# Kernel tuning notes

Hardware: AMD Instinct MI355X
Metric: run time of the kernel (lower is better)

Reference implementation:

```python
import jax, jax.numpy as jnp
import numpy as np


def setup_inputs() -> dict:
    key = jax.random.key(0)
    k0, k1, k2, k3, k4 = jax.random.split(key, 5)
    B, S, D, F, E = 2, 1024, 1024, 2048, 8
    x = jax.random.normal(k0, (B, S, D), dtype=jnp.float32)
    router_weight = jax.random.normal(k1, (D, E), dtype=jnp.float32) * (1.0 / np.sqrt(D))
    std_in = (1.0 / np.sqrt(3.0)) / np.sqrt(D)   # fan_in = d_model for w1/w2
    std_out = (1.0 / np.sqrt(3.0)) / np.sqrt(F)  # fan_in = d_ff for w3
    w1 = jax.random.normal(k2, (E, D, F), dtype=jnp.float32) * std_in
    w2 = jax.random.normal(k3, (E, D, F), dtype=jnp.float32) * std_in
    w3 = jax.random.normal(k4, (E, F, D), dtype=jnp.float32) * std_out
    return {"x": x, "router_weight": router_weight, "w1": w1, "w2": w2, "w3": w3, "top_k": 2}


def reference(x, router_weight, w1, w2, w3, top_k):
    B, S, D = x.shape
    E = w1.shape[0]
    xf = x.reshape(-1, D)                         # (T, D), T = B*S
    T = xf.shape[0]
    # Router: linear + softmax + top-k, then renormalize top-k weights
    logits = xf @ router_weight                   # (T, E)
    probs = jax.nn.softmax(logits, axis=-1)
    topk_w, topk_idx = jax.lax.top_k(probs, top_k)  # (T, k)
    topk_w = topk_w / jnp.sum(topk_w, axis=-1, keepdims=True)
    # Dense combine weights: cw[t, e] = routing weight if expert e selected for token t, else 0
    cw = jnp.zeros((T, E), dtype=xf.dtype).at[jnp.arange(T)[:, None], topk_idx].add(topk_w)
    # Expert SwiGLU: loop over small fixed expert count (structurally distinct weights)
    out = jnp.zeros_like(xf)
    for e in range(E):
        h = jax.nn.silu(xf @ w1[e]) * (xf @ w2[e])  # (T, F)
        out = out + cw[:, e:e + 1] * (h @ w3[e])    # (T, D)
    return out.reshape(B, S, D)
```

## Files before the change

kernel.cpp:

```cpp
#include <hip/hip_runtime.h>
#include <hip/hip_bf16.h>
#include <stdint.h>

#define T_TOK 2048
#define DMODEL 1024
#define FDIM 2048
#define NEXP 8
#define MAXS 40

typedef __bf16 bf16;
typedef __attribute__((ext_vector_type(8))) __bf16 bf16x8;
typedef __attribute__((ext_vector_type(4))) float f32x4;

#define GLOBAL_AS __attribute__((address_space(1)))
#define LDS_AS __attribute__((address_space(3)))
#define VMCNT(n) asm volatile("s_waitcnt vmcnt(" #n ")" ::: "memory")
#define GLD16(src, dst) __builtin_amdgcn_global_load_lds((const GLOBAL_AS void*)(src), (LDS_AS void*)(dst), 16, 0, 0)

#define XG_SLOT   131072u
#define H_SLOT    262144u
#define W_SLAB    2097152u

__global__ __launch_bounds__(64) void moe_router(
    const float* __restrict__ x, const float* __restrict__ rw,
    bf16* __restrict__ xb, int* __restrict__ counts,
    int* __restrict__ tok_list, float* __restrict__ wgt_list)
{
  const int t = blockIdx.x;
  const int lane = threadIdx.x;
  const float* xr = x + (size_t)t * DMODEL;
  float acc[NEXP];
#pragma unroll
  for (int e = 0; e < NEXP; ++e) acc[e] = 0.f;
  for (int d = lane; d < DMODEL; d += 64) {
    float xv = xr[d];
    if (xb) xb[(size_t)t * DMODEL + d] = (bf16)xv;
    const float* r = rw + (size_t)d * NEXP;
#pragma unroll
    for (int e = 0; e < NEXP; ++e) acc[e] += xv * r[e];
  }
#pragma unroll
  for (int e = 0; e < NEXP; ++e) {
#pragma unroll
    for (int off = 32; off >= 1; off >>= 1)
      acc[e] += __shfl_xor(acc[e], off, 64);
  }
  if (lane == 0) {
    int i0 = 0; float m0 = acc[0];
#pragma unroll
    for (int e = 1; e < NEXP; ++e) { if (acc[e] > m0) { m0 = acc[e]; i0 = e; } }
    int i1 = -1; float m1 = -3.402823466e38f;
#pragma unroll
    for (int e = 0; e < NEXP; ++e) { if (e != i0 && acc[e] > m1) { m1 = acc[e]; i1 = e; } }
    float r = expf(m1 - m0);
    float w0 = 1.f / (1.f + r);
    float w1v = r / (1.f + r);
    int p0 = atomicAdd(&counts[i0], 1);
    tok_list[i0 * T_TOK + p0] = t;
    wgt_list[i0 * T_TOK + p0] = w0;
    int p1 = atomicAdd(&counts[i1], 1);
    tok_list[i1 * T_TOK + p1] = t;
    wgt_list[i1 * T_TOK + p1] = w1v;
  }
}

__global__ void moe_prefix(const int* __restrict__ counts, int* __restrict__ base,
                           int* __restrict__ sched)
{
  if (threadIdx.x == 0) {
    int s = 0, i = 0;
    for (int e = 0; e < NEXP; ++e) {
      base[e] = s; s += counts[e];
      const int nt = (counts[e] + 127) / 128;
      for (int tt = 0; tt < nt; ++tt) sched[i++] = (e << 16) | tt;
    }
    for (; i < MAXS; ++i) sched[i] = -1;
  }
}

__global__ __launch_bounds__(256) void moe_gather(
    const float* __restrict__ x, const int* __restrict__ tok_list,
    const int* __restrict__ counts, const int* __restrict__ sched,
    bf16* __restrict__ xg)
{
  const int s = sched[blockIdx.x];
  if (s < 0) return;
  const int e = s >> 16, tt = s & 0xffff;
  int rem = counts[e] - tt * 128; if (rem > 128) rem = 128;
  const int w = threadIdx.x >> 6, lane = threadIdx.x & 63;
  const int r = blockIdx.y * 4 + w;
  const int rc = r < rem ? r : rem - 1;
  const int tok = tok_list[e * T_TOK + tt * 128 + rc];
  const float* xr = x + (size_t)tok * DMODEL + lane * 16;
  f32x4 v0 = *(const f32x4*)(xr);
  f32x4 v1 = *(const f32x4*)(xr + 4);
  f32x4 v2 = *(const f32x4*)(xr + 8);
  f32x4 v3 = *(const f32x4*)(xr + 12);
  bf16x8 a, b;
#pragma unroll
  for (int j = 0; j < 4; ++j) { a[j] = (bf16)v0[j]; a[4 + j] = (bf16)v1[j]; }
#pragma unroll
  for (int j = 0; j < 4; ++j) { b[j] = (bf16)v2[j]; b[4 + j] = (bf16)v3[j]; }
  bf16* dst = xg + (size_t)blockIdx.x * XG_SLOT + (size_t)(lane * 2) * 1024 + r * 8;
  *(bf16x8*)dst = a;
  *(bf16x8*)(dst + 1024) = b;
}

__global__ __launch_bounds__(256) void transpose_blk12(
    const float* __restrict__ w1, const float* __restrict__ w2,
    bf16* __restrict__ w1b, bf16* __restrict__ w2b)
{
  const int C = FDIM;
  __shared__ float tile[64][65];
  const int z = blockIdx.z;
  const int e = z & 7;
  const float* inp = (z < 8 ? w1 : w2) + (size_t)e * DMODEL * FDIM;
  bf16* outp = (z < 8 ? w1b : w2b) + (size_t)e * W_SLAB;
  const int rb = blockIdx.y * 64;
  const int cb = blockIdx.x * 64;
  const int tid = threadIdx.x;
  const int r = tid >> 2, c0 = (tid & 3) * 16;
  const float* src = inp + (size_t)(rb + r) * C + (cb + c0);
#pragma unroll
  for (int j = 0; j < 16; j += 4) {
    f32x4 v = *(const f32x4*)(src + j);
    tile[r][c0 + j + 0] = v[0];
    tile[r][c0 + j + 1] = v[1];
    tile[r][c0 + j + 2] = v[2];
    tile[r][c0 + j + 3] = v[3];
  }
  __syncthreads();
  bf16x8 a, b;
#pragma unroll
  for (int j = 0; j < 8; ++j) a[j] = (bf16)tile[c0 + j][r];
#pragma unroll
  for (int j = 0; j < 8; ++j) b[j] = (bf16)tile[c0 + 8 + j][r];
  const int ft = blockIdx.x;
  const int ktd = blockIdx.y * 2 + c0 / 32;
  const int kc = (c0 & 31) / 8;
  bf16* dst = outp + ((size_t)ft * 128 + ktd * 4 + kc) * 512 + r * 8;
  *(bf16x8*)dst = a;
  *(bf16x8*)(dst + 512) = b;
}

__global__ __launch_bounds__(256) void transpose_blk3(
    const float* __restrict__ w3, bf16* __restrict__ w3b)
{
  const int C = DMODEL;
  __shared__ float tile[64][65];
  const int e = blockIdx.z;
  const float* inp = w3 + (size_t)e * FDIM * DMODEL;
  bf16* outp = w3b + (size_t)e * W_SLAB;
  const int rb = blockIdx.y * 64;
  const int cb = blockIdx.x * 64;
  const int tid = threadIdx.x;
  const int r = tid >> 2, c0 = (tid & 3) * 16;
  const float* src = inp + (size_t)(rb + r) * C + (cb + c0);
#pragma unroll
  for (int j = 0; j < 16; j += 4) {
    f32x4 v = *(const f32x4*)(src + j);
    tile[r][c0 + j + 0] = v[0];
    tile[r][c0 + j + 1] = v[1];
    tile[r][c0 + j + 2] = v[2];
    tile[r][c0 + j + 3] = v[3];
  }
  __syncthreads();
  bf16x8 a, b;
#pragma unroll
  for (int j = 0; j < 8; ++j) a[j] = (bf16)tile[c0 + j][r];
#pragma unroll
  for (int j = 0; j < 8; ++j) b[j] = (bf16)tile[c0 + 8 + j][r];
  const int dt = blockIdx.x;
  const int ktf = blockIdx.y * 2 + c0 / 32;
  const int kc = (c0 & 31) / 8;
  bf16* dst = outp + ((size_t)dt * 256 + ktf * 4 + kc) * 512 + r * 8;
  *(bf16x8*)dst = a;
  *(bf16x8*)(dst + 512) = b;
}

__global__ __launch_bounds__(256) void moe_gemm1_blk(
    const bf16* __restrict__ xg,
    const bf16* __restrict__ w1b, const bf16* __restrict__ w2b,
    const int* __restrict__ counts, const int* __restrict__ sched,
    bf16* __restrict__ hblk)
{
  const int s = sched[blockIdx.y];
  if (s < 0) return;
  const int e = s >> 16, tt = s & 0xffff;
  int rem = counts[e] - tt * 128; if (rem > 128) rem = 128;
  const int ft = blockIdx.x;

  __shared__ __align__(16) bf16 As[3][4][128][8];
  __shared__ __align__(16) bf16 Ws[3][2][4][64][8];

  const int tid = threadIdx.x;
  const int lane = tid & 63;
  const int w = tid >> 6;
  const int wr = w >> 1, wc = w & 1;
  const int lh = lane >> 4, ll = lane & 15;

  const bf16* axg = xg + (size_t)blockIdx.y * XG_SLOT + w * 1024 + lane * 8;
  const bf16* w1e = w1b + (size_t)e * W_SLAB + ((size_t)ft * 128 + w) * 512 + lane * 8;
  const bf16* w2e = w2b + (size_t)e * W_SLAB + ((size_t)ft * 128 + w) * 512 + lane * 8;

  f32x4 acc1[4][2], acc2[4][2];
  const f32x4 fz = {0.f, 0.f, 0.f, 0.f};
#pragma unroll
  for (int mf = 0; mf < 4; ++mf)
#pragma unroll
    for (int nf = 0; nf < 2; ++nf) { acc1[mf][nf] = fz; acc2[mf][nf] = fz; }

#define STAGE1(B, KT)                                              \
  {                                                                \
    GLD16(axg + (size_t)(KT) * 4096,       &As[B][w][0][0]);       \
    GLD16(axg + (size_t)(KT) * 4096 + 512, &As[B][w][64][0]);      \
    GLD16(w1e + (size_t)(KT) * 2048,       &Ws[B][0][w][0][0]);    \
    GLD16(w2e + (size_t)(KT) * 2048,       &Ws[B][1][w][0][0]);    \
  }

  const int NT = DMODEL / 32;
  STAGE1(0, 0);
  STAGE1(1, 1);
  VMCNT(4);
  __builtin_amdgcn_s_barrier();

  int ld = 0;
  for (int t = 0; t < NT; ++t) {
    int pf = ld + 2; if (pf >= 3) pf -= 3;
    if (t + 2 < NT) STAGE1(pf, t + 2);

    bf16x8 af[4], b1[2], b2[2];
#pragma unroll
    for (int mf = 0; mf < 4; ++mf)
      af[mf] = *(const bf16x8*)&As[ld][lh][wr * 64 + mf * 16 + ll][0];
#pragma unroll
    for (int nf = 0; nf < 2; ++nf) {
      b1[nf] = *(const bf16x8*)&Ws[ld][0][lh][wc * 32 + nf * 16 + ll][0];
      b2[nf] = *(const bf16x8*)&Ws[ld][1][lh][wc * 32 + nf * 16 + ll][0];
    }
    __builtin_amdgcn_s_setprio(1);
#pragma unroll
    for (int mf = 0; mf < 4; ++mf)
#pragma unroll
      for (int nf = 0; nf < 2; ++nf) {
        acc1[mf][nf] = __builtin_amdgcn_mfma_f32_16x16x32_bf16(af[mf], b1[nf], acc1[mf][nf], 0, 0, 0);
        acc2[mf][nf] = __builtin_amdgcn_mfma_f32_16x16x32_bf16(af[mf], b2[nf], acc2[mf][nf], 0, 0, 0);
      }
    __builtin_amdgcn_s_setprio(0);

    if (t + 2 < NT)      { VMCNT(4); __builtin_amdgcn_s_barrier(); }
    else if (t + 1 < NT) { VMCNT(0); __builtin_amdgcn_s_barrier(); }
    ld = (ld + 1 == 3) ? 0 : ld + 1;
  }
#undef STAGE1

  bf16* hs = hblk + (size_t)blockIdx.y * H_SLOT;
  const int kth = ft * 2 + wc;
#pragma unroll
  for (int mf = 0; mf < 4; ++mf)
#pragma unroll
    for (int nf = 0; nf < 2; ++nf) {
      const int kch = nf * 2 + (ll >> 3);
      bf16* hp = hs + ((size_t)kth * 4 + kch) * 1024 + (ll & 7);
#pragma unroll
      for (int r = 0; r < 4; ++r) {
        const int rl = wr * 64 + mf * 16 + lh * 4 + r;
        if (rl < rem) {
          const float a = acc1[mf][nf][r];
          const float b = acc2[mf][nf][r];
          const float h = (a / (1.f + expf(-a))) * b;
          hp[rl * 8] = (bf16)h;
        }
      }
    }
}

__global__ __launch_bounds__(256) void moe_gemm2_blk(
    const bf16* __restrict__ hblk, const bf16* __restrict__ w3b,
    const int* __restrict__ tok_list, const float* __restrict__ wgt_list,
    const int* __restrict__ counts, const int* __restrict__ sched,
    float* __restrict__ out)
{
  const int s = sched[blockIdx.y];
  if (s < 0) return;
  const int e = s >> 16, tt = s & 0xffff;
  int rem = counts[e] - tt * 128; if (rem > 128) rem = 128;
  const int dtb = blockIdx.x;
  const int kz = blockIdx.z;

  __shared__ __align__(16) bf16 As[3][4][128][8];
  __shared__ __align__(16) bf16 Ws[3][4][128][8];
  __shared__ int toks[128];
  __shared__ float wgts[128];

  const int tid = threadIdx.x;
  const int lane = tid & 63;
  const int w = tid >> 6;
  const int wr = w >> 1, wc = w & 1;
  const int lh = lane >> 4, ll = lane & 15;

  if (tid < 128) {
    int r = tid < rem ? tid : rem - 1;
    toks[tid] = tok_list[e * T_TOK + tt * 128 + r];
    wgts[tid] = wgt_list[e * T_TOK + tt * 128 + r];
  }
  __syncthreads();

  const bf16* ah = hblk + (size_t)blockIdx.y * H_SLOT + (size_t)kz * 131072 + w * 1024 + lane * 8;
  const int fh = w & 1;
  const int kcp = (w >> 1) << 1;
  const bf16* w3w = w3b + (size_t)e * W_SLAB
      + ((size_t)(2 * dtb + fh) * 256 + (size_t)kz * 128 + kcp) * 512 + lane * 8;

  f32x4 acc[4][4];
  const f32x4 fz = {0.f, 0.f, 0.f, 0.f};
#pragma unroll
  for (int mf = 0; mf < 4; ++mf)
#pragma unroll
    for (int nf = 0; nf < 4; ++nf) acc[mf][nf] = fz;

#define STAGE2(B, KT)                                                    \
  {                                                                      \
    GLD16(ah  + (size_t)(KT) * 4096,       &As[B][w][0][0]);             \
    GLD16(ah  + (size_t)(KT) * 4096 + 512, &As[B][w][64][0]);            \
    GLD16(w3w + (size_t)(KT) * 2048,       &Ws[B][kcp][fh * 64][0]);     \
    GLD16(w3w + (size_t)(KT) * 2048 + 512, &Ws[B][kcp + 1][fh * 64][0]); \
  }

  const int NT = (FDIM / 2) / 32;
  STAGE2(0, 0);
  STAGE2(1, 1);
  VMCNT(4);
  __builtin_amdgcn_s_barrier();

  int ld = 0;
  for (int t = 0; t < NT; ++t) {
    int pf = ld + 2; if (pf >= 3) pf -= 3;
    if (t + 2 < NT) STAGE2(pf, t + 2);

    bf16x8 af[4], bv[4];
#pragma unroll
    for (int mf = 0; mf < 4; ++mf)
      af[mf] = *(const bf16x8*)&As[ld][lh][wr * 64 + mf * 16 + ll][0];
#pragma unroll
    for (int nf = 0; nf < 4; ++nf)
      bv[nf] = *(const bf16x8*)&Ws[ld][lh][wc * 64 + nf * 16 + ll][0];
    __builtin_amdgcn_s_setprio(1);
#pragma unroll
    for (int mf = 0; mf < 4; ++mf)
#pragma unroll
      for (int nf = 0; nf < 4; ++nf)
        acc[mf][nf] = __builtin_amdgcn_mfma_f32_16x16x32_bf16(af[mf], bv[nf], acc[mf][nf], 0, 0, 0);
    __builtin_amdgcn_s_setprio(0);

    if (t + 2 < NT)      { VMCNT(4); __builtin_amdgcn_s_barrier(); }
    else if (t + 1 < NT) { VMCNT(0); __builtin_amdgcn_s_barrier(); }
    ld = (ld + 1 == 3) ? 0 : ld + 1;
  }
#undef STAGE2

#pragma unroll
  for (int mf = 0; mf < 4; ++mf)
#pragma unroll
    for (int nf = 0; nf < 4; ++nf)
#pragma unroll
      for (int r = 0; r < 4; ++r) {
        const int rl = wr * 64 + mf * 16 + lh * 4 + r;
        if (rl < rem) {
          const int col = dtb * 128 + wc * 64 + nf * 16 + ll;
          atomicAdd(&out[(size_t)toks[rl] * DMODEL + col], acc[mf][nf][r] * wgts[rl]);
        }
      }
}

__global__ __launch_bounds__(256, 2) void moe_gemm1(
    const bf16* __restrict__ xb,
    const float* __restrict__ w1, const float* __restrict__ w2,
    const int* __restrict__ tok_list, const int* __restrict__ counts,
    const int* __restrict__ base, bf16* __restrict__ H)
{
  const int e = blockIdx.z;
  const int tt = blockIdx.y;
  const int ft = blockIdx.x;
  const int cnt = counts[e];
  if (tt * 128 >= cnt) return;
  int rem = cnt - tt * 128; if (rem > 128) rem = 128;

  __shared__ __align__(16) bf16 As[4][128][8];
  __shared__ __align__(16) bf16 Ws[2][4][64][8];
  __shared__ int toks[128];

  const int tid = threadIdx.x;
  const int lane = tid & 63;
  const int w = tid >> 6;
  const int wr = w >> 1, wc = w & 1;
  const int lh = lane >> 4, ll = lane & 15;

  if (tid < 128) {
    int r = tid < rem ? tid : rem - 1;
    toks[tid] = tok_list[e * T_TOK + tt * 128 + r];
  }
  __syncthreads();

  f32x4 acc1[4][2], acc2[4][2];
  const f32x4 fz = {0.f, 0.f, 0.f, 0.f};
#pragma unroll
  for (int mf = 0; mf < 4; ++mf)
#pragma unroll
    for (int nf = 0; nf < 2; ++nf) { acc1[mf][nf] = fz; acc2[mf][nf] = fz; }

  const float* w1e = w1 + (size_t)e * DMODEL * FDIM + ft * 64;
  const float* w2e = w2 + (size_t)e * DMODEL * FDIM + ft * 64;
  const int sf = tid & 63;
  const int skc = tid >> 6;

  for (int k0 = 0; k0 < DMODEL; k0 += 32) {
    __syncthreads();
#pragma unroll
    for (int i = 0; i < 2; ++i) {
      const int c = w + i * 4;
      const int kc = c >> 1;
      const int rh = c & 1;
      const int row = rh * 64 + lane;
      GLD16(xb + (size_t)toks[row] * DMODEL + (k0 + kc * 8), &As[kc][rh * 64][0]);
    }
    {
      const size_t rowoff = (size_t)(k0 + skc * 8) * FDIM + sf;
      const float* s1 = w1e + rowoff;
      const float* s2 = w2e + rowoff;
      bf16x8 v1, v2;
#pragma unroll
      for (int j = 0; j < 8; ++j) {
        v1[j] = (bf16)s1[(size_t)j * FDIM];
        v2[j] = (bf16)s2[(size_t)j * FDIM];
      }
      *(bf16x8*)&Ws[0][skc][sf][0] = v1;
      *(bf16x8*)&Ws[1][skc][sf][0] = v2;
    }
    __syncthreads();
    bf16x8 af[4];
#pragma unroll
    for (int mf = 0; mf < 4; ++mf)
      af[mf] = *(const bf16x8*)&As[lh][wr * 64 + mf * 16 + ll][0];
    bf16x8 b1[2], b2[2];
#pragma unroll
    for (int nf = 0; nf < 2; ++nf) {
      b1[nf] = *(const bf16x8*)&Ws[0][lh][wc * 32 + nf * 16 + ll][0];
      b2[nf] = *(const bf16x8*)&Ws[1][lh][wc * 32 + nf * 16 + ll][0];
    }
#pragma unroll
    for (int mf = 0; mf < 4; ++mf)
#pragma unroll
      for (int nf = 0; nf < 2; ++nf) {
        acc1[mf][nf] = __builtin_amdgcn_mfma_f32_16x16x32_bf16(af[mf], b1[nf], acc1[mf][nf], 0, 0, 0);
        acc2[mf][nf] = __builtin_amdgcn_mfma_f32_16x16x32_bf16(af[mf], b2[nf], acc2[mf][nf], 0, 0, 0);
      }
  }

  const int hbase = base[e] + tt * 128;
#pragma unroll
  for (int mf = 0; mf < 4; ++mf)
#pragma unroll
    for (int nf = 0; nf < 2; ++nf)
#pragma unroll
      for (int r = 0; r < 4; ++r) {
        const int rl = wr * 64 + mf * 16 + lh * 4 + r;
        if (rl < rem) {
          const int fg = ft * 64 + wc * 32 + nf * 16 + ll;
          const float a = acc1[mf][nf][r];
          const float b = acc2[mf][nf][r];
          const float h = (a / (1.f + expf(-a))) * b;
          H[(size_t)(hbase + rl) * FDIM + fg] = (bf16)h;
        }
      }
}

__global__ __launch_bounds__(256, 2) void moe_gemm2(
    const bf16* __restrict__ H, const float* __restrict__ w3,
    const int* __restrict__ tok_list, const float* __restrict__ wgt_list,
    const int* __restrict__ counts, const int* __restrict__ base,
    float* __restrict__ out)
{
  const int e = blockIdx.z;
  const int tt = blockIdx.y;
  const int dt = blockIdx.x;
  const int cnt = counts[e];
  if (tt * 128 >= cnt) return;
  int rem = cnt - tt * 128; if (rem > 128) rem = 128;

  __shared__ __align__(16) bf16 As[4][128][8];
  __shared__ __align__(16) bf16 Ws[4][64][8];
  __shared__ int toks[128];
  __shared__ float wgts[128];

  const int tid = threadIdx.x;
  const int lane = tid & 63;
  const int w = tid >> 6;
  const int wr = w >> 1, wc = w & 1;
  const int lh = lane >> 4, ll = lane & 15;

  if (tid < 128) {
    int r = tid < rem ? tid : rem - 1;
    toks[tid] = tok_list[e * T_TOK + tt * 128 + r];
    wgts[tid] = wgt_list[e * T_TOK + tt * 128 + r];
  }
  __syncthreads();

  f32x4 acc[4][2];
  const f32x4 fz = {0.f, 0.f, 0.f, 0.f};
#pragma unroll
  for (int mf = 0; mf < 4; ++mf)
#pragma unroll
    for (int nf = 0; nf < 2; ++nf) acc[mf][nf] = fz;

  const int hbase = base[e] + tt * 128;
  const float* w3e = w3 + (size_t)e * FDIM * DMODEL + dt * 64;
  const int sf = tid & 63;
  const int skc = tid >> 6;

  for (int k0 = 0; k0 < FDIM; k0 += 32) {
    __syncthreads();
#pragma unroll
    for (int i = 0; i < 2; ++i) {
      const int c = w + i * 4;
      const int kc = c >> 1;
      const int rh = c & 1;
      int row = rh * 64 + lane;
      if (row >= rem) row = rem - 1;
      GLD16(H + (size_t)(hbase + row) * FDIM + (k0 + kc * 8), &As[kc][rh * 64][0]);
    }
    {
      const size_t rowoff = (size_t)(k0 + skc * 8) * DMODEL + sf;
      const float* s3 = w3e + rowoff;
      bf16x8 v;
#pragma unroll
      for (int j = 0; j < 8; ++j) v[j] = (bf16)s3[(size_t)j * DMODEL];
      *(bf16x8*)&Ws[skc][sf][0] = v;
    }
    __syncthreads();
    bf16x8 af[4];
#pragma unroll
    for (int mf = 0; mf < 4; ++mf)
      af[mf] = *(const bf16x8*)&As[lh][wr * 64 + mf * 16 + ll][0];
    bf16x8 bv[2];
#pragma unroll
    for (int nf = 0; nf < 2; ++nf)
      bv[nf] = *(const bf16x8*)&Ws[lh][wc * 32 + nf * 16 + ll][0];
#pragma unroll
    for (int mf = 0; mf < 4; ++mf)
#pragma unroll
      for (int nf = 0; nf < 2; ++nf)
        acc[mf][nf] = __builtin_amdgcn_mfma_f32_16x16x32_bf16(af[mf], bv[nf], acc[mf][nf], 0, 0, 0);
  }

#pragma unroll
  for (int mf = 0; mf < 4; ++mf)
#pragma unroll
    for (int nf = 0; nf < 2; ++nf)
#pragma unroll
      for (int r = 0; r < 4; ++r) {
        const int rl = wr * 64 + mf * 16 + lh * 4 + r;
        if (rl < rem) {
          const int col = dt * 64 + wc * 32 + nf * 16 + ll;
          atomicAdd(&out[(size_t)toks[rl] * DMODEL + col], acc[mf][nf][r] * wgts[rl]);
        }
      }
}

extern "C" void kernel_launch(void* const* d_in, const int* in_sizes, int n_in,
                              void* d_out, int out_size, void* d_ws, size_t ws_size,
                              hipStream_t stream)
{
  const float* x  = (const float*)d_in[0];
  const float* rw = (const float*)d_in[1];
  const float* w1 = (const float*)d_in[2];
  const float* w2 = (const float*)d_in[3];
  const float* w3 = (const float*)d_in[4];
  float* out = (float*)d_out;
  char* ws = (char*)d_ws;

  size_t off = 0;
  auto take = [&](size_t bytes) -> char* {
    char* p = ws + off;
    off = (off + bytes + 255) & ~(size_t)255;
    return p;
  };
  int* tok_list   = (int*)take((size_t)NEXP * T_TOK * sizeof(int));
  float* wgt_list = (float*)take((size_t)NEXP * T_TOK * sizeof(float));
  int* counts     = (int*)take(64);
  int* base       = (int*)take(64);
  int* sched      = (int*)take(MAXS * sizeof(int));
  bf16* xg        = (bf16*)take((size_t)MAXS * XG_SLOT * sizeof(bf16));
  bf16* hblk      = (bf16*)take((size_t)MAXS * H_SLOT * sizeof(bf16));
  bf16* w1b       = (bf16*)take((size_t)NEXP * W_SLAB * sizeof(bf16));
  bf16* w2b       = (bf16*)take((size_t)NEXP * W_SLAB * sizeof(bf16));
  bf16* w3b       = (bf16*)take((size_t)NEXP * W_SLAB * sizeof(bf16));
  const bool fast = (ws_size >= off);

  hipMemsetAsync(d_out, 0, (size_t)out_size * sizeof(float), stream);
  hipMemsetAsync(counts, 0, NEXP * sizeof(int), stream);

  if (fast) {
    moe_router<<<dim3(T_TOK), dim3(64), 0, stream>>>(x, rw, nullptr, counts, tok_list, wgt_list);
    moe_prefix<<<dim3(1), dim3(64), 0, stream>>>(counts, base, sched);
    transpose_blk12<<<dim3(FDIM / 64, DMODEL / 64, 2 * NEXP), dim3(256), 0, stream>>>(w1, w2, w1b, w2b);
    transpose_blk3<<<dim3(DMODEL / 64, FDIM / 64, NEXP), dim3(256), 0, stream>>>(w3, w3b);
    moe_gather<<<dim3(MAXS, 32), dim3(256), 0, stream>>>(x, tok_list, counts, sched, xg);
    moe_gemm1_blk<<<dim3(FDIM / 64, MAXS), dim3(256), 0, stream>>>(
        xg, w1b, w2b, counts, sched, hblk);
    moe_gemm2_blk<<<dim3(DMODEL / 128, MAXS, 2), dim3(256), 0, stream>>>(
        hblk, w3b, tok_list, wgt_list, counts, sched, out);
  } else {
    size_t foff = 0;
    auto ftake = [&](size_t bytes) -> char* {
      char* p = ws + foff;
      foff = (foff + bytes + 255) & ~(size_t)255;
      return p;
    };
    int* ftok   = (int*)ftake((size_t)NEXP * T_TOK * sizeof(int));
    float* fwgt = (float*)ftake((size_t)NEXP * T_TOK * sizeof(float));
    int* fcnt   = (int*)ftake(64);
    int* fbase  = (int*)ftake(64);
    int* fsched = (int*)ftake(MAXS * sizeof(int));
    bf16* xb    = (bf16*)ftake((size_t)T_TOK * DMODEL * sizeof(bf16));
    bf16* H     = (bf16*)ftake((size_t)2 * T_TOK * FDIM * sizeof(bf16));
    hipMemsetAsync(fcnt, 0, NEXP * sizeof(int), stream);
    moe_router<<<dim3(T_TOK), dim3(64), 0, stream>>>(x, rw, xb, fcnt, ftok, fwgt);
    moe_prefix<<<dim3(1), dim3(64), 0, stream>>>(fcnt, fbase, fsched);
    moe_gemm1<<<dim3(FDIM / 64, T_TOK / 128, NEXP), dim3(256), 0, stream>>>(
        xb, w1, w2, ftok, fcnt, fbase, H);
    moe_gemm2<<<dim3(DMODEL / 64, T_TOK / 128, NEXP), dim3(256), 0, stream>>>(
        H, w3, ftok, fwgt, fcnt, fbase, out);
  }
}
```

Measured before the change: 245.8 us.

## Fuse fp32 weight conversion into GEMM kernels, drop separate transpose passes

Removes the two transpose/convert kernels that rewrote all expert weights into a blocked bf16 layout every call. Instead, each GEMM block loads fp32 weight tiles into registers, converts them to bf16 and writes them into a swizzled, padded LDS buffer that is double-buffered alongside the async activation loads. This avoids a full read/write pass over roughly 200MB of weights and two launches. The cost is that each weight tile is now read as fp32 (twice the bytes) by every token tile that uses it, and B fragments are gathered from LDS as scalar bf16 loads instead of vector loads.

Measured after the change: 292.3 us. 18.9% more time.

```diff
diff --git a/kernel.cpp b/kernel.cpp
--- a/kernel.cpp
+++ b/kernel.cpp
@@ -15,11 +15,11 @@
 #define GLOBAL_AS __attribute__((address_space(1)))
 #define LDS_AS __attribute__((address_space(3)))
 #define VMCNT(n) asm volatile("s_waitcnt vmcnt(" #n ")" ::: "memory")
+#define LGKM0    asm volatile("s_waitcnt lgkmcnt(0)" ::: "memory")
 #define GLD16(src, dst) __builtin_amdgcn_global_load_lds((const GLOBAL_AS void*)(src), (LDS_AS void*)(dst), 16, 0, 0)
 
 #define XG_SLOT   131072u
 #define H_SLOT    262144u
-#define W_SLAB    2097152u
 
 __global__ __launch_bounds__(64) void moe_router(
     const float* __restrict__ x, const float* __restrict__ rw,
@@ -106,81 +106,9 @@
   *(bf16x8*)(dst + 1024) = b;
 }
 
-__global__ __launch_bounds__(256) void transpose_blk12(
-    const float* __restrict__ w1, const float* __restrict__ w2,
-    bf16* __restrict__ w1b, bf16* __restrict__ w2b)
-{
-  const int C = FDIM;
-  __shared__ float tile[64][65];
-  const int z = blockIdx.z;
-  const int e = z & 7;
-  const float* inp = (z < 8 ? w1 : w2) + (size_t)e * DMODEL * FDIM;
-  bf16* outp = (z < 8 ? w1b : w2b) + (size_t)e * W_SLAB;
-  const int rb = blockIdx.y * 64;
-  const int cb = blockIdx.x * 64;
-  const int tid = threadIdx.x;
-  const int r = tid >> 2, c0 = (tid & 3) * 16;
-  const float* src = inp + (size_t)(rb + r) * C + (cb + c0);
-#pragma unroll
-  for (int j = 0; j < 16; j += 4) {
-    f32x4 v = *(const f32x4*)(src + j);
-    tile[r][c0 + j + 0] = v[0];
-    tile[r][c0 + j + 1] = v[1];
-    tile[r][c0 + j + 2] = v[2];
-    tile[r][c0 + j + 3] = v[3];
-  }
-  __syncthreads();
-  bf16x8 a, b;
-#pragma unroll
-  for (int j = 0; j < 8; ++j) a[j] = (bf16)tile[c0 + j][r];
-#pragma unroll
-  for (int j = 0; j < 8; ++j) b[j] = (bf16)tile[c0 + 8 + j][r];
-  const int ft = blockIdx.x;
-  const int ktd = blockIdx.y * 2 + c0 / 32;
-  const int kc = (c0 & 31) / 8;
-  bf16* dst = outp + ((size_t)ft * 128 + ktd * 4 + kc) * 512 + r * 8;
-  *(bf16x8*)dst = a;
-  *(bf16x8*)(dst + 512) = b;
-}
-
-__global__ __launch_bounds__(256) void transpose_blk3(
-    const float* __restrict__ w3, bf16* __restrict__ w3b)
-{
-  const int C = DMODEL;
-  __shared__ float tile[64][65];
-  const int e = blockIdx.z;
-  const float* inp = w3 + (size_t)e * FDIM * DMODEL;
-  bf16* outp = w3b + (size_t)e * W_SLAB;
-  const int rb = blockIdx.y * 64;
-  const int cb = blockIdx.x * 64;
-  const int tid = threadIdx.x;
-  const int r = tid >> 2, c0 = (tid & 3) * 16;
-  const float* src = inp + (size_t)(rb + r) * C + (cb + c0);
-#pragma unroll
-  for (int j = 0; j < 16; j += 4) {
-    f32x4 v = *(const f32x4*)(src + j);
-    tile[r][c0 + j + 0] = v[0];
-    tile[r][c0 + j + 1] = v[1];
-    tile[r][c0 + j + 2] = v[2];
-    tile[r][c0 + j + 3] = v[3];
-  }
-  __syncthreads();
-  bf16x8 a, b;
-#pragma unroll
-  for (int j = 0; j < 8; ++j) a[j] = (bf16)tile[c0 + j][r];
-#pragma unroll
-  for (int j = 0; j < 8; ++j) b[j] = (bf16)tile[c0 + 8 + j][r];
-  const int dt = blockIdx.x;
-  const int ktf = blockIdx.y * 2 + c0 / 32;
-  const int kc = (c0 & 31) / 8;
-  bf16* dst = outp + ((size_t)dt * 256 + ktf * 4 + kc) * 512 + r * 8;
-  *(bf16x8*)dst = a;
-  *(bf16x8*)(dst + 512) = b;
-}
-
 __global__ __launch_bounds__(256) void moe_gemm1_blk(
     const bf16* __restrict__ xg,
-    const bf16* __restrict__ w1b, const bf16* __restrict__ w2b,
+    const float* __restrict__ w1, const float* __restrict__ w2,
     const int* __restrict__ counts, const int* __restrict__ sched,
     bf16* __restrict__ hblk)
 {
@@ -191,7 +119,7 @@
   const int ft = blockIdx.x;
 
   __shared__ __align__(16) bf16 As[3][4][128][8];
-  __shared__ __align__(16) bf16 Ws[3][2][4][64][8];
+  __shared__ __align__(16) bf16 Wraw[2][2][32][72];
 
   const int tid = threadIdx.x;
   const int lane = tid & 63;
@@ -200,8 +128,15 @@
   const int lh = lane >> 4, ll = lane & 15;
 
   const bf16* axg = xg + (size_t)blockIdx.y * XG_SLOT + w * 1024 + lane * 8;
-  const bf16* w1e = w1b + (size_t)e * W_SLAB + ((size_t)ft * 128 + w) * 512 + lane * 8;
-  const bf16* w2e = w2b + (size_t)e * W_SLAB + ((size_t)ft * 128 + w) * 512 + lane * 8;
+
+  const int wm  = tid >> 7;
+  const int wrk = (tid & 127) >> 2;
+  const int wfc = (tid & 3) << 4;
+  const int wfx = wfc ^ ((wrk >> 3) << 4);
+  const float* wsrc = (wm ? w2 : w1) + (size_t)e * DMODEL * FDIM
+      + (size_t)wrk * FDIM + ft * 64 + wfc;
+
+  f32x4 wv0, wv1, wv2, wv3;
 
   f32x4 acc1[4][2], acc2[4][2];
   const f32x4 fz = {0.f, 0.f, 0.f, 0.f};
@@ -210,49 +145,78 @@
 #pragma unroll
     for (int nf = 0; nf < 2; ++nf) { acc1[mf][nf] = fz; acc2[mf][nf] = fz; }
 
-#define STAGE1(B, KT)                                              \
-  {                                                                \
-    GLD16(axg + (size_t)(KT) * 4096,       &As[B][w][0][0]);       \
-    GLD16(axg + (size_t)(KT) * 4096 + 512, &As[B][w][64][0]);      \
-    GLD16(w1e + (size_t)(KT) * 2048,       &Ws[B][0][w][0][0]);    \
-    GLD16(w2e + (size_t)(KT) * 2048,       &Ws[B][1][w][0][0]);    \
+#define WISSUE1(KT)                                                  \
+  {                                                                  \
+    const float* p_ = wsrc + (size_t)(KT) * (32 * FDIM);             \
+    wv0 = *(const f32x4*)p_;        wv1 = *(const f32x4*)(p_ + 4);   \
+    wv2 = *(const f32x4*)(p_ + 8);  wv3 = *(const f32x4*)(p_ + 12);  \
+  }
+#define WWRITE1(B)                                                   \
+  {                                                                  \
+    bf16x8 lo_, hi_;                                                 \
+    _Pragma("unroll") for (int j = 0; j < 4; ++j) {                  \
+      lo_[j] = (bf16)wv0[j]; lo_[4 + j] = (bf16)wv1[j];              \
+      hi_[j] = (bf16)wv2[j]; hi_[4 + j] = (bf16)wv3[j];              \
+    }                                                                \
+    bf16* d_ = &Wraw[B][wm][wrk][wfx];                               \
+    *(bf16x8*)d_ = lo_;  *(bf16x8*)(d_ + 8) = hi_;                   \
+  }
+#define STAGEA1(B, KT)                                               \
+  {                                                                  \
+    GLD16(axg + (size_t)(KT) * 4096,       &As[B][w][0][0]);         \
+    GLD16(axg + (size_t)(KT) * 4096 + 512, &As[B][w][64][0]);        \
+  }
+#define COMPUTE1(LA, LW)                                                         \
+  {                                                                              \
+    bf16x8 af[4], b1v[2], b2v[2];                                                \
+    _Pragma("unroll") for (int mf = 0; mf < 4; ++mf)                             \
+      af[mf] = *(const bf16x8*)&As[LA][lh][wr * 64 + mf * 16 + ll][0];           \
+    _Pragma("unroll") for (int nf = 0; nf < 2; ++nf) {                           \
+      const int fp_ = (((wc << 1) | nf) ^ lh) * 16 + ll;                         \
+      _Pragma("unroll") for (int j = 0; j < 8; ++j) {                            \
+        b1v[nf][j] = Wraw[LW][0][8 * lh + j][fp_];                               \
+        b2v[nf][j] = Wraw[LW][1][8 * lh + j][fp_];                               \
+      }                                                                          \
+    }                                                                            \
+    __builtin_amdgcn_s_setprio(1);                                               \
+    _Pragma("unroll") for (int mf = 0; mf < 4; ++mf)                             \
+      _Pragma("unroll") for (int nf = 0; nf < 2; ++nf) {                         \
+        acc1[mf][nf] = __builtin_amdgcn_mfma_f32_16x16x32_bf16(af[mf], b1v[nf], acc1[mf][nf], 0, 0, 0); \
+        acc2[mf][nf] = __builtin_amdgcn_mfma_f32_16x16x32_bf16(af[mf], b2v[nf], acc2[mf][nf], 0, 0, 0); \
+      }                                                                          \
+    __builtin_amdgcn_s_setprio(0);                                               \
   }
 
   const int NT = DMODEL / 32;
-  STAGE1(0, 0);
-  STAGE1(1, 1);
-  VMCNT(4);
+  WISSUE1(0);
+  STAGEA1(0, 0);
+  STAGEA1(1, 1);
+  VMCNT(2);
+  WWRITE1(0);
+  LGKM0;
   __builtin_amdgcn_s_barrier();
 
   int ld = 0;
   for (int t = 0; t < NT; ++t) {
+    if (t + 1 < NT) WISSUE1(t + 1);
     int pf = ld + 2; if (pf >= 3) pf -= 3;
-    if (t + 2 < NT) STAGE1(pf, t + 2);
-
-    bf16x8 af[4], b1[2], b2[2];
-#pragma unroll
-    for (int mf = 0; mf < 4; ++mf)
-      af[mf] = *(const bf16x8*)&As[ld][lh][wr * 64 + mf * 16 + ll][0];
-#pragma unroll
-    for (int nf = 0; nf < 2; ++nf) {
-      b1[nf] = *(const bf16x8*)&Ws[ld][0][lh][wc * 32 + nf * 16 + ll][0];
-      b2[nf] = *(const bf16x8*)&Ws[ld][1][lh][wc * 32 + nf * 16 + ll][0];
-    }
-    __builtin_amdgcn_s_setprio(1);
-#pragma unroll
-    for (int mf = 0; mf < 4; ++mf)
-#pragma unroll
-      for (int nf = 0; nf < 2; ++nf) {
-        acc1[mf][nf] = __builtin_amdgcn_mfma_f32_16x16x32_bf16(af[mf], b1[nf], acc1[mf][nf], 0, 0, 0);
-        acc2[mf][nf] = __builtin_amdgcn_mfma_f32_16x16x32_bf16(af[mf], b2[nf], acc2[mf][nf], 0, 0, 0);
-      }
-    __builtin_amdgcn_s_setprio(0);
-
-    if (t + 2 < NT)      { VMCNT(4); __builtin_amdgcn_s_barrier(); }
-    else if (t + 1 < NT) { VMCNT(0); __builtin_amdgcn_s_barrier(); }
+    if (t + 2 < NT) STAGEA1(pf, t + 2);
+
+    COMPUTE1(ld, t & 1);
+
+    if (t + 2 < NT)      { VMCNT(2); }
+    else if (t + 1 < NT) { VMCNT(0); }
+    if (t + 1 < NT) {
+      WWRITE1((t + 1) & 1);
+      LGKM0;
+      __builtin_amdgcn_s_barrier();
+    }
     ld = (ld + 1 == 3) ? 0 : ld + 1;
   }
-#undef STAGE1
+#undef WISSUE1
+#undef WWRITE1
+#undef STAGEA1
+#undef COMPUTE1
 
   bf16* hs = hblk + (size_t)blockIdx.y * H_SLOT;
   const int kth = ft * 2 + wc;
@@ -276,7 +240,7 @@
 }
 
 __global__ __launch_bounds__(256) void moe_gemm2_blk(
-    const bf16* __restrict__ hblk, const bf16* __restrict__ w3b,
+    const bf16* __restrict__ hblk, const float* __restrict__ w3,
     const int* __restrict__ tok_list, const float* __restrict__ wgt_list,
     const int* __restrict__ counts, const int* __restrict__ sched,
     float* __restrict__ out)
@@ -289,7 +253,7 @@
   const int kz = blockIdx.z;
 
   __shared__ __align__(16) bf16 As[3][4][128][8];
-  __shared__ __align__(16) bf16 Ws[3][4][128][8];
+  __shared__ __align__(16) bf16 Wraw[2][32][136];
   __shared__ int toks[128];
   __shared__ float wgts[128];
 
@@ -307,10 +271,14 @@
   __syncthreads();
 
   const bf16* ah = hblk + (size_t)blockIdx.y * H_SLOT + (size_t)kz * 131072 + w * 1024 + lane * 8;
-  const int fh = w & 1;
-  const int kcp = (w >> 1) << 1;
-  const bf16* w3w = w3b + (size_t)e * W_SLAB
-      + ((size_t)(2 * dtb + fh) * 256 + (size_t)kz * 128 + kcp) * 512 + lane * 8;
+
+  const int wrk = tid >> 3;
+  const int wfc = (tid & 7) << 4;
+  const int wfx = wfc ^ ((wrk >> 3) << 4);
+  const float* wsrc = w3 + (size_t)e * FDIM * DMODEL
+      + (size_t)(kz * (FDIM / 2) + wrk) * DMODEL + dtb * 128 + wfc;
+
+  f32x4 wv0, wv1, wv2, wv3;
 
   f32x4 acc[4][4];
   const f32x4 fz = {0.f, 0.f, 0.f, 0.f};
@@ -319,45 +287,74 @@
 #pragma unroll
     for (int nf = 0; nf < 4; ++nf) acc[mf][nf] = fz;
 
-#define STAGE2(B, KT)                                                    \
-  {                                                                      \
-    GLD16(ah  + (size_t)(KT) * 4096,       &As[B][w][0][0]);             \
-    GLD16(ah  + (size_t)(KT) * 4096 + 512, &As[B][w][64][0]);            \
-    GLD16(w3w + (size_t)(KT) * 2048,       &Ws[B][kcp][fh * 64][0]);     \
-    GLD16(w3w + (size_t)(KT) * 2048 + 512, &Ws[B][kcp + 1][fh * 64][0]); \
+#define WISSUE2(KT)                                                  \
+  {                                                                  \
+    const float* p_ = wsrc + (size_t)(KT) * (32 * DMODEL);           \
+    wv0 = *(const f32x4*)p_;        wv1 = *(const f32x4*)(p_ + 4);   \
+    wv2 = *(const f32x4*)(p_ + 8);  wv3 = *(const f32x4*)(p_ + 12);  \
+  }
+#define WWRITE2(B)                                                   \
+  {                                                                  \
+    bf16x8 lo_, hi_;                                                 \
+    _Pragma("unroll") for (int j = 0; j < 4; ++j) {                  \
+      lo_[j] = (bf16)wv0[j]; lo_[4 + j] = (bf16)wv1[j];              \
+      hi_[j] = (bf16)wv2[j]; hi_[4 + j] = (bf16)wv3[j];              \
+    }                                                                \
+    bf16* d_ = &Wraw[B][wrk][wfx];                                   \
+    *(bf16x8*)d_ = lo_;  *(bf16x8*)(d_ + 8) = hi_;                   \
+  }
+#define STAGEA2(B, KT)                                               \
+  {                                                                  \
+    GLD16(ah + (size_t)(KT) * 4096,       &As[B][w][0][0]);          \
+    GLD16(ah + (size_t)(KT) * 4096 + 512, &As[B][w][64][0]);         \
+  }
+#define COMPUTE2(LA, LW)                                                         \
+  {                                                                              \
+    bf16x8 af[4], bv[4];                                                         \
+    _Pragma("unroll") for (int mf = 0; mf < 4; ++mf)                             \
+      af[mf] = *(const bf16x8*)&As[LA][lh][wr * 64 + mf * 16 + ll][0];           \
+    _Pragma("unroll") for (int nf = 0; nf < 4; ++nf) {                           \
+      const int fp_ = (((wc << 2) | nf) ^ lh) * 16 + ll;                         \
+      _Pragma("unroll") for (int j = 0; j < 8; ++j)                              \
+        bv[nf][j] = Wraw[LW][8 * lh + j][fp_];                                   \
+    }                                                                            \
+    __builtin_amdgcn_s_setprio(1);                                               \
+    _Pragma("unroll") for (int mf = 0; mf < 4; ++mf)                             \
+      _Pragma("unroll") for (int nf = 0; nf < 4; ++nf)                           \
+        acc[mf][nf] = __builtin_amdgcn_mfma_f32_16x16x32_bf16(af[mf], bv[nf], acc[mf][nf], 0, 0, 0); \
+    __builtin_amdgcn_s_setprio(0);                                               \
   }
 
   const int NT = (FDIM / 2) / 32;
-  STAGE2(0, 0);
-  STAGE2(1, 1);
-  VMCNT(4);
+  WISSUE2(0);
+  STAGEA2(0, 0);
+  STAGEA2(1, 1);
+  VMCNT(2);
+  WWRITE2(0);
+  LGKM0;
   __builtin_amdgcn_s_barrier();
 
   int ld = 0;
   for (int t = 0; t < NT; ++t) {
+    if (t + 1 < NT) WISSUE2(t + 1);
     int pf = ld + 2; if (pf >= 3) pf -= 3;
-    if (t + 2 < NT) STAGE2(pf, t + 2);
-
-    bf16x8 af[4], bv[4];
-#pragma unroll
-    for (int mf = 0; mf < 4; ++mf)
-      af[mf] = *(const bf16x8*)&As[ld][lh][wr * 64 + mf * 16 + ll][0];
-#pragma unroll
-    for (int nf = 0; nf < 4; ++nf)
-      bv[nf] = *(const bf16x8*)&Ws[ld][lh][wc * 64 + nf * 16 + ll][0];
-    __builtin_amdgcn_s_setprio(1);
-#pragma unroll
-    for (int mf = 0; mf < 4; ++mf)
-#pragma unroll
-      for (int nf = 0; nf < 4; ++nf)
-        acc[mf][nf] = __builtin_amdgcn_mfma_f32_16x16x32_bf16(af[mf], bv[nf], acc[mf][nf], 0, 0, 0);
-    __builtin_amdgcn_s_setprio(0);
-
-    if (t + 2 < NT)      { VMCNT(4); __builtin_amdgcn_s_barrier(); }
-    else if (t + 1 < NT) { VMCNT(0); __builtin_amdgcn_s_barrier(); }
+    if (t + 2 < NT) STAGEA2(pf, t + 2);
+
+    COMPUTE2(ld, t & 1);
+
+    if (t + 2 < NT)      { VMCNT(2); }
+    else if (t + 1 < NT) { VMCNT(0); }
+    if (t + 1 < NT) {
+      WWRITE2((t + 1) & 1);
+      LGKM0;
+      __builtin_amdgcn_s_barrier();
+    }
     ld = (ld + 1 == 3) ? 0 : ld + 1;
   }
-#undef STAGE2
+#undef WISSUE2
+#undef WWRITE2
+#undef STAGEA2
+#undef COMPUTE2
 
 #pragma unroll
   for (int mf = 0; mf < 4; ++mf)
@@ -592,9 +589,6 @@
   int* sched      = (int*)take(MAXS * sizeof(int));
   bf16* xg        = (bf16*)take((size_t)MAXS * XG_SLOT * sizeof(bf16));
   bf16* hblk      = (bf16*)take((size_t)MAXS * H_SLOT * sizeof(bf16));
-  bf16* w1b       = (bf16*)take((size_t)NEXP * W_SLAB * sizeof(bf16));
-  bf16* w2b       = (bf16*)take((size_t)NEXP * W_SLAB * sizeof(bf16));
-  bf16* w3b       = (bf16*)take((size_t)NEXP * W_SLAB * sizeof(bf16));
   const bool fast = (ws_size >= off);
 
   hipMemsetAsync(d_out, 0, (size_t)out_size * sizeof(float), stream);
@@ -603,13 +597,11 @@
   if (fast) {
     moe_router<<<dim3(T_TOK), dim3(64), 0, stream>>>(x, rw, nullptr, counts, tok_list, wgt_list);
     moe_prefix<<<dim3(1), dim3(64), 0, stream>>>(counts, base, sched);
-    transpose_blk12<<<dim3(FDIM / 64, DMODEL / 64, 2 * NEXP), dim3(256), 0, stream>>>(w1, w2, w1b, w2b);
-    transpose_blk3<<<dim3(DMODEL / 64, FDIM / 64, NEXP), dim3(256), 0, stream>>>(w3, w3b);
     moe_gather<<<dim3(MAXS, 32), dim3(256), 0, stream>>>(x, tok_list, counts, sched, xg);
     moe_gemm1_blk<<<dim3(FDIM / 64, MAXS), dim3(256), 0, stream>>>(
-        xg, w1b, w2b, counts, sched, hblk);
+        xg, w1, w2, counts, sched, hblk);
     moe_gemm2_blk<<<dim3(DMODEL / 128, MAXS, 2), dim3(256), 0, stream>>>(
-        hblk, w3b, tok_list, wgt_list, counts, sched, out);
+        hblk, w3, tok_list, wgt_list, counts, sched, out);
   } else {
     size_t foff = 0;
     auto ftake = [&](size_t bytes) -> char* {
```

## Enlarge gemm1 token tile to 256 rows with 512-thread blocks

Applied to the files above, without the earlier changes.

Adds a second schedule that pairs adjacent 128-token tiles of the same expert into 256-token tiles. The gate/up GEMM now runs 8 waves per block over 256 rows, so each w1/w2 slab is loaded from memory once per 256 tokens instead of once per 128. This is meant to halve weight traffic and cut the block count for that kernel. In exchange it needs more LDS per block and has fewer, larger blocks, which may lower occupancy and worsen load balance across CUs.

New measurement: 250.7 us. 1.02x slower.

```diff
diff --git a/kernel.cpp b/kernel.cpp
--- a/kernel.cpp
+++ b/kernel.cpp
@@ -7,6 +7,7 @@
 #define FDIM 2048
 #define NEXP 8
 #define MAXS 40
+#define MAXS2 24
 
 typedef __bf16 bf16;
 typedef __attribute__((ext_vector_type(8))) __bf16 bf16x8;
@@ -65,16 +66,29 @@
 }
 
 __global__ void moe_prefix(const int* __restrict__ counts, int* __restrict__ base,
-                           int* __restrict__ sched)
+                           int* __restrict__ sched, int* __restrict__ sched256)
 {
   if (threadIdx.x == 0) {
+    int sstart[NEXP];
     int s = 0, i = 0;
     for (int e = 0; e < NEXP; ++e) {
       base[e] = s; s += counts[e];
+      sstart[e] = i;
       const int nt = (counts[e] + 127) / 128;
       for (int tt = 0; tt < nt; ++tt) sched[i++] = (e << 16) | tt;
     }
-    for (; i < MAXS; ++i) sched[i] = -1;
+    for (int k = i; k < MAXS; ++k) sched[k] = -1;
+    int i2 = 0;
+    for (int e = 0; e < NEXP; ++e) {
+      const int nt128 = (counts[e] + 127) / 128;
+      const int nt256 = (counts[e] + 255) / 256;
+      for (int j = 0; j < nt256; ++j) {
+        const int lo = sstart[e] + 2 * j;
+        const int hi = (2 * j + 1 < nt128) ? lo + 1 : lo;
+        sched256[i2++] = (e << 28) | (j << 24) | (lo << 8) | hi;
+      }
+    }
+    for (int k = i2; k < MAXS2; ++k) sched256[k] = -1;
   }
 }
 
@@ -178,19 +192,20 @@
   *(bf16x8*)(dst + 512) = b;
 }
 
-__global__ __launch_bounds__(256) void moe_gemm1_blk(
+__global__ __launch_bounds__(512) void moe_gemm1_blk(
     const bf16* __restrict__ xg,
     const bf16* __restrict__ w1b, const bf16* __restrict__ w2b,
-    const int* __restrict__ counts, const int* __restrict__ sched,
+    const int* __restrict__ counts, const int* __restrict__ sched256,
     bf16* __restrict__ hblk)
 {
-  const int s = sched[blockIdx.y];
+  const int s = sched256[blockIdx.y];
   if (s < 0) return;
-  const int e = s >> 16, tt = s & 0xffff;
-  int rem = counts[e] - tt * 128; if (rem > 128) rem = 128;
+  const int e = (s >> 28) & 7, t256 = (s >> 24) & 15;
+  const int sLo = (s >> 8) & 0xff, sHi = s & 0xff;
+  int rem = counts[e] - t256 * 256; if (rem > 256) rem = 256;
   const int ft = blockIdx.x;
 
-  __shared__ __align__(16) bf16 As[3][4][128][8];
+  __shared__ __align__(16) bf16 As[3][4][256][8];
   __shared__ __align__(16) bf16 Ws[3][2][4][64][8];
 
   const int tid = threadIdx.x;
@@ -199,9 +214,13 @@
   const int wr = w >> 1, wc = w & 1;
   const int lh = lane >> 4, ll = lane & 15;
 
-  const bf16* axg = xg + (size_t)blockIdx.y * XG_SLOT + w * 1024 + lane * 8;
-  const bf16* w1e = w1b + (size_t)e * W_SLAB + ((size_t)ft * 128 + w) * 512 + lane * 8;
-  const bf16* w2e = w2b + (size_t)e * W_SLAB + ((size_t)ft * 128 + w) * 512 + lane * 8;
+  const int c0 = 2 * w, c1 = 2 * w + 1;
+  const int kc0 = c0 >> 2, q0 = c0 & 3;
+  const int kc1 = c1 >> 2, q1 = c1 & 3;
+  const bf16* asrc0 = xg + (size_t)(q0 >= 2 ? sHi : sLo) * XG_SLOT + kc0 * 1024 + (q0 & 1) * 512 + lane * 8;
+  const bf16* asrc1 = xg + (size_t)(q1 >= 2 ? sHi : sLo) * XG_SLOT + kc1 * 1024 + (q1 & 1) * 512 + lane * 8;
+  const int wm = w >> 2, wkc = w & 3;
+  const bf16* wsrc = (wm ? w2b : w1b) + (size_t)e * W_SLAB + ((size_t)ft * 128 + wkc) * 512 + lane * 8;
 
   f32x4 acc1[4][2], acc2[4][2];
   const f32x4 fz = {0.f, 0.f, 0.f, 0.f};
@@ -212,16 +231,15 @@
 
 #define STAGE1(B, KT)                                              \
   {                                                                \
-    GLD16(axg + (size_t)(KT) * 4096,       &As[B][w][0][0]);       \
-    GLD16(axg + (size_t)(KT) * 4096 + 512, &As[B][w][64][0]);      \
-    GLD16(w1e + (size_t)(KT) * 2048,       &Ws[B][0][w][0][0]);    \
-    GLD16(w2e + (size_t)(KT) * 2048,       &Ws[B][1][w][0][0]);    \
+    GLD16(asrc0 + (size_t)(KT) * 4096, &As[B][kc0][q0 * 64][0]);   \
+    GLD16(asrc1 + (size_t)(KT) * 4096, &As[B][kc1][q1 * 64][0]);   \
+    GLD16(wsrc  + (size_t)(KT) * 2048, &Ws[B][wm][wkc][0][0]);     \
   }
 
   const int NT = DMODEL / 32;
   STAGE1(0, 0);
   STAGE1(1, 1);
-  VMCNT(4);
+  VMCNT(3);
   __builtin_amdgcn_s_barrier();
 
   int ld = 0;
@@ -248,28 +266,27 @@
       }
     __builtin_amdgcn_s_setprio(0);
 
-    if (t + 2 < NT)      { VMCNT(4); __builtin_amdgcn_s_barrier(); }
+    if (t + 2 < NT)      { VMCNT(3); __builtin_amdgcn_s_barrier(); }
     else if (t + 1 < NT) { VMCNT(0); __builtin_amdgcn_s_barrier(); }
     ld = (ld + 1 == 3) ? 0 : ld + 1;
   }
 #undef STAGE1
 
-  bf16* hs = hblk + (size_t)blockIdx.y * H_SLOT;
   const int kth = ft * 2 + wc;
 #pragma unroll
   for (int mf = 0; mf < 4; ++mf)
 #pragma unroll
     for (int nf = 0; nf < 2; ++nf) {
       const int kch = nf * 2 + (ll >> 3);
-      bf16* hp = hs + ((size_t)kth * 4 + kch) * 1024 + (ll & 7);
 #pragma unroll
       for (int r = 0; r < 4; ++r) {
         const int rl = wr * 64 + mf * 16 + lh * 4 + r;
         if (rl < rem) {
+          bf16* hs = hblk + (size_t)(rl < 128 ? sLo : sHi) * H_SLOT;
           const float a = acc1[mf][nf][r];
           const float b = acc2[mf][nf][r];
           const float h = (a / (1.f + expf(-a))) * b;
-          hp[rl * 8] = (bf16)h;
+          hs[((size_t)kth * 4 + kch) * 1024 + (size_t)(rl & 127) * 8 + (ll & 7)] = (bf16)h;
         }
       }
     }
@@ -590,6 +607,7 @@
   int* counts     = (int*)take(64);
   int* base       = (int*)take(64);
   int* sched      = (int*)take(MAXS * sizeof(int));
+  int* sched256   = (int*)take(MAXS2 * sizeof(int));
   bf16* xg        = (bf16*)take((size_t)MAXS * XG_SLOT * sizeof(bf16));
   bf16* hblk      = (bf16*)take((size_t)MAXS * H_SLOT * sizeof(bf16));
   bf16* w1b       = (bf16*)take((size_t)NEXP * W_SLAB * sizeof(bf16));
@@ -602,12 +620,12 @@
 
   if (fast) {
     moe_router<<<dim3(T_TOK), dim3(64), 0, stream>>>(x, rw, nullptr, counts, tok_list, wgt_list);
-    moe_prefix<<<dim3(1), dim3(64), 0, stream>>>(counts, base, sched);
+    moe_prefix<<<dim3(1), dim3(64), 0, stream>>>(counts, base, sched, sched256);
     transpose_blk12<<<dim3(FDIM / 64, DMODEL / 64, 2 * NEXP), dim3(256), 0, stream>>>(w1, w2, w1b, w2b);
     transpose_blk3<<<dim3(DMODEL / 64, FDIM / 64, NEXP), dim3(256), 0, stream>>>(w3, w3b);
     moe_gather<<<dim3(MAXS, 32), dim3(256), 0, stream>>>(x, tok_list, counts, sched, xg);
-    moe_gemm1_blk<<<dim3(FDIM / 64, MAXS), dim3(256), 0, stream>>>(
-        xg, w1b, w2b, counts, sched, hblk);
+    moe_gemm1_blk<<<dim3(FDIM / 64, MAXS2), dim3(512), 0, stream>>>(
+        xg, w1b, w2b, counts, sched256, hblk);
     moe_gemm2_blk<<<dim3(DMODEL / 128, MAXS, 2), dim3(256), 0, stream>>>(
         hblk, w3b, tok_list, wgt_list, counts, sched, out);
   } else {
@@ -622,11 +640,12 @@
     int* fcnt   = (int*)ftake(64);
     int* fbase  = (int*)ftake(64);
     int* fsched = (int*)ftake(MAXS * sizeof(int));
+    int* fs256  = (int*)ftake(MAXS2 * sizeof(int));
     bf16* xb    = (bf16*)ftake((size_t)T_TOK * DMODEL * sizeof(bf16));
     bf16* H     = (bf16*)ftake((size_t)2 * T_TOK * FDIM * sizeof(bf16));
     hipMemsetAsync(fcnt, 0, NEXP * sizeof(int), stream);
     moe_router<<<dim3(T_TOK), dim3(64), 0, stream>>>(x, rw, xb, fcnt, ftok, fwgt);
-    moe_prefix<<<dim3(1), dim3(64), 0, stream>>>(fcnt, fbase, fsched);
+    moe_prefix<<<dim3(1), dim3(64), 0, stream>>>(fcnt, fbase, fsched, fs256);
     moe_gemm1<<<dim3(FDIM / 64, T_TOK / 128, NEXP), dim3(256), 0, stream>>>(
         xb, w1, w2, ftok, fcnt, fbase, H);
     moe_gemm2<<<dim3(DMODEL / 64, T_TOK / 128, NEXP), dim3(256), 0, stream>>>(
```
